# Performance work log

Hardware: AMD Instinct MI355X
Metric: run time of the kernel (lower is better)

## Reference

```python
import jax, jax.numpy as jnp
import numpy as np

VOCAB = 32000
D_MODEL = 768
D_FF = 3072
N_LAYERS = 12
SEQ = 2048
BATCH = 8
EPS = 1e-5  # torch LayerNorm default


def _layernorm(x, g, b):
    mu = jnp.mean(x, axis=-1, keepdims=True)
    var = jnp.mean(jnp.square(x - mu), axis=-1, keepdims=True)
    return (x - mu) * jax.lax.rsqrt(var + EPS) * g + b


def setup_inputs() -> dict:
    key = jax.random.key(0)
    ks = jax.random.split(key, 12)
    tokens = jax.random.randint(ks[0], (BATCH, SEQ), 0, VOCAB)
    embed = jax.random.normal(ks[1], (VOCAB, D_MODEL), dtype=jnp.float32) * 0.02
    ln1_g = jnp.ones((N_LAYERS, D_MODEL), dtype=jnp.float32)
    ln1_b = jnp.zeros((N_LAYERS, D_MODEL), dtype=jnp.float32)
    ln2_g = jnp.ones((N_LAYERS, D_MODEL), dtype=jnp.float32)
    ln2_b = jnp.zeros((N_LAYERS, D_MODEL), dtype=jnp.float32)
    W1 = jax.random.normal(ks[2], (N_LAYERS, D_MODEL, D_FF), dtype=jnp.float32) * (1.0 / np.sqrt(D_MODEL))
    b1 = jnp.zeros((N_LAYERS, D_FF), dtype=jnp.float32)
    W2 = jax.random.normal(ks[3], (N_LAYERS, D_FF, D_MODEL), dtype=jnp.float32) * (1.0 / np.sqrt(D_FF))
    b2 = jnp.zeros((N_LAYERS, D_MODEL), dtype=jnp.float32)
    Wout = jax.random.normal(ks[4], (D_MODEL, VOCAB), dtype=jnp.float32) * (1.0 / np.sqrt(D_MODEL))
    bout = jnp.zeros((VOCAB,), dtype=jnp.float32)
    return {"tokens": tokens, "embed": embed, "ln1_g": ln1_g, "ln1_b": ln1_b,
            "ln2_g": ln2_g, "ln2_b": ln2_b, "W1": W1, "b1": b1, "W2": W2, "b2": b2,
            "Wout": Wout, "bout": bout}


def reference(tokens, embed, ln1_g, ln1_b, ln2_g, ln2_b, W1, b1, W2, b2, Wout, bout):
    # embedding lookup; embed_size == d_model so projection is Identity.
    x = embed[tokens]  # [B, S, D]
    # dropout is inference-mode identity
    for l in range(N_LAYERS):
        res = x
        h = _layernorm(x, ln1_g[l], ln1_b[l])
        h = jnp.fft.fft2(h, axes=(-2, -1)).real  # token mixing, keep real part
        x = h + res
        res = x
        h = _layernorm(x, ln2_g[l], ln2_b[l])
        h = jax.nn.gelu(jnp.einsum('bsd,df->bsf', h, W1[l]) + b1[l], approximate=False)
        h = jnp.einsum('bsf,fd->bsd', h, W2[l]) + b2[l]
        x = h + res
    # predict from last position
    return jnp.einsum('bd,dv->bv', x[:, -1, :], Wout) + bout
```

## Files before the change

kernel.cpp:

```cpp
#include <hip/hip_runtime.h>
#include <hip/hip_bf16.h>

typedef unsigned short u16;
typedef unsigned long long u64;
typedef __attribute__((ext_vector_type(8))) __bf16 bf16x8;
typedef __attribute__((ext_vector_type(4))) float f32x4;
typedef __attribute__((ext_vector_type(4))) unsigned short u16x4;

#define BB 8
#define SS 2048
#define DD 768
#define DFF 3072
#define NL 12
#define ROWS (BB*SS)
#define VOC 32000

__device__ __forceinline__ u16 f2bf(float f){
  union { float f; unsigned u; } v; v.f = f;
  unsigned u = v.u;
  u += 0x7FFF + ((u >> 16) & 1);
  return (u16)(u >> 16);
}
__device__ __forceinline__ float bf2f(u16 b){
  union { unsigned u; float f; } v; v.u = ((unsigned)b) << 16; return v.f;
}

__global__ void k_embed(const int* __restrict__ tok, const float4* __restrict__ emb,
                        float4* __restrict__ x){
  int i = blockIdx.x*256 + threadIdx.x;
  if (i >= ROWS*192) return;
  int row = i/192, c = i - row*192;
  x[i] = emb[(long)tok[row]*192 + c];
}

__global__ void k_dftD(u16* __restrict__ out){
  int i = blockIdx.x*256 + threadIdx.x;
  if (i >= 1536*768) return;
  int n = i/768, k = i - n*768;
  int nn = (n < 768) ? n : n - 768;
  int m = (nn*k) % 768;
  float a = 2.0f*(float)m/768.0f;
  out[i] = f2bf((n < 768) ? cospif(a) : sinpif(a));
}

__global__ void k_dftS2(u16* __restrict__ out){
  int i = blockIdx.x*256 + threadIdx.x;
  if (i >= 2048*2048) return;
  int t = i >> 11, slot = i & 2047;
  int ss = (slot <= 1024) ? slot : slot - 1024;
  int m = (t*ss) & 2047;
  float a = (float)m * (1.0f/1024.0f);
  out[i] = f2bf((slot <= 1024) ? cospif(a) : -sinpif(a));
}

template<bool RES>
__global__ void k_ln1_fold(float* __restrict__ x, const u16* __restrict__ t4,
                           const float* __restrict__ bias,
                           const float* __restrict__ g, const float* __restrict__ b,
                           u16* __restrict__ hp, u16* __restrict__ hm){
  int gid = blockIdx.x*4 + (threadIdx.x >> 6);
  if (gid >= 8*1025) return;
  int bb = gid/1025, t = gid - bb*1025;
  int u = (2048 - t) & 2047;
  long rt = (long)bb*2048 + t, ru = (long)bb*2048 + u;
  int lane = threadIdx.x & 63;
  float vt[12], vu[12];
  #pragma unroll
  for (int j = 0; j < 12; j++){
    int e = lane + j*64;
    float a0 = x[rt*DD + e], a1 = x[ru*DD + e];
    if (RES){
      float bv = bias[e];
      a0 += bf2f(t4[rt*DD + e]) + bv;
      a1 += bf2f(t4[ru*DD + e]) + bv;
    }
    vt[j] = a0; vu[j] = a1;
  }
  float s0 = 0.f, s1 = 0.f;
  #pragma unroll
  for (int j = 0; j < 12; j++){ s0 += vt[j]; s1 += vu[j]; }
  #pragma unroll
  for (int o = 32; o > 0; o >>= 1){ s0 += __shfl_xor(s0, o); s1 += __shfl_xor(s1, o); }
  float mu0 = s0*(1.0f/768.0f), mu1 = s1*(1.0f/768.0f);
  float q0 = 0.f, q1 = 0.f;
  #pragma unroll
  for (int j = 0; j < 12; j++){ float d0 = vt[j]-mu0, d1 = vu[j]-mu1; q0 += d0*d0; q1 += d1*d1; }
  #pragma unroll
  for (int o = 32; o > 0; o >>= 1){ q0 += __shfl_xor(q0, o); q1 += __shfl_xor(q1, o); }
  float r0 = rsqrtf(q0*(1.0f/768.0f) + 1e-5f);
  float r1 = rsqrtf(q1*(1.0f/768.0f) + 1e-5f);
  const bool single = (t == 0) || (t == 1024);
  u16* hpr = hp + ((long)bb*1280 + t)*DD;
  u16* hmr = hm + ((long)bb*1024 + t)*DD;
  #pragma unroll
  for (int j = 0; j < 12; j++){
    int e = lane + j*64;
    if (RES){ x[rt*DD + e] = vt[j]; x[ru*DD + e] = vu[j]; }
    float ht = (vt[j]-mu0)*r0*g[e] + b[e];
    float hu = (vu[j]-mu1)*r1*g[e] + b[e];
    hpr[e] = f2bf(single ? ht : ht + hu);
    if (!single) hmr[e] = f2bf(ht - hu);
  }
}

__global__ void k_ln2_fuse(float* __restrict__ x, const u16* __restrict__ t2,
                           const float* __restrict__ g, const float* __restrict__ b,
                           u16* __restrict__ h){
  long row = (long)blockIdx.x*4 + (threadIdx.x >> 6);
  int lane = threadIdx.x & 63;
  float v[12];
  float s = 0.f;
  #pragma unroll
  for (int j = 0; j < 12; j++){
    int e = lane + j*64;
    float a = x[row*DD + e] + bf2f(t2[row*DD + e]);
    v[j] = a; s += a;
  }
  #pragma unroll
  for (int o = 32; o > 0; o >>= 1) s += __shfl_xor(s, o);
  float mu = s * (1.0f/768.0f);
  float q = 0.f;
  #pragma unroll
  for (int j = 0; j < 12; j++){ float d = v[j]-mu; q += d*d; }
  #pragma unroll
  for (int o = 32; o > 0; o >>= 1) q += __shfl_xor(q, o);
  float rs = rsqrtf(q * (1.0f/768.0f) + 1e-5f);
  #pragma unroll
  for (int j = 0; j < 12; j++){
    int e = lane + j*64;
    x[row*DD + e] = v[j];
    h[row*DD + e] = f2bf((v[j]-mu)*rs*g[e] + b[e]);
  }
}

__global__ void k_transpose_cvt(const float* __restrict__ src, u16* __restrict__ dst,
                                int R, int C){
  __shared__ float t[32][33];
  int bx = blockIdx.x*32, by = blockIdx.y*32;
  int tx = threadIdx.x, ty = threadIdx.y;
  #pragma unroll
  for (int i = 0; i < 4; i++) t[ty+i*8][tx] = src[(long)(by+ty+i*8)*C + bx+tx];
  __syncthreads();
  #pragma unroll
  for (int i = 0; i < 4; i++) dst[(long)(bx+ty+i*8)*R + by+tx] = f2bf(t[tx][ty+i*8]);
}

#define EPI_ADDX 1
#define EPI_GELU 2
#define EPI_OUTB 3

#define MFMA_Q(H, G, BF) do { \
  __builtin_amdgcn_s_setprio(1); \
  _Pragma("unroll") \
  for (int mm = 0; mm < 4; ++mm) \
    _Pragma("unroll") \
    for (int nn = 0; nn < 2; ++nn) \
      _Pragma("unroll") \
      for (int ks = 0; ks < 2; ++ks) \
        acc[((H)<<2)+mm][((G)<<1)+nn] = __builtin_amdgcn_mfma_f32_16x16x32_bf16( \
            aF[mm][ks], BF[nn][ks], acc[((H)<<2)+mm][((G)<<1)+nn], 0, 0, 0); \
  __builtin_amdgcn_s_setprio(0); \
} while(0)

#define GEMM_CORE_BODY \
  f32x4 acc[8][4] = {}; \
  bf16x8 aF[4][2], b0F[2][2], b1F[2][2]; \
  auto stage = [&](int tile){ \
    if (tile >= NT) return; \
    _Pragma("unroll") \
    for (int hh = 0; hh < 4; ++hh){ \
      const int isB   = ((hh + 1) >> 1) & 1; \
      const int rhalf = ((hh >> 1) & 1) << 7; \
      const u16* src = isB ? Bb : Ab; \
      const int rb = (isB ? bn : bm) + rhalf + sRow; \
      const u16* s0 = src + (long)rb * K + (tile << 6) + sCol; \
      u16* d0 = &lds[tile & 1][isB][rhalf + (wave << 3)][0]; \
      __builtin_amdgcn_global_load_lds((__attribute__((address_space(1))) void*)(s0), \
                                       (__attribute__((address_space(3))) void*)(d0), 16, 0, 0); \
      __builtin_amdgcn_global_load_lds((__attribute__((address_space(1))) void*)(s0 + ((long)K << 6)), \
                                       (__attribute__((address_space(3))) void*)(d0 + 64*64), 16, 0, 0); \
    } \
  }; \
  auto readA = [&](int c, int H){ \
    const u16* base = &lds[c][0][(H << 7) + (wm << 6)][0]; \
    _Pragma("unroll") \
    for (int mm = 0; mm < 4; ++mm) \
      _Pragma("unroll") \
      for (int ks = 0; ks < 2; ++ks) \
        aF[mm][ks] = *(const bf16x8*)&base[((mm<<4) + fr)*64 + (((ks<<5) + fks8) ^ swz)]; \
  }; \
  auto readB = [&](int c, int G, bf16x8 (&bF)[2][2]){ \
    const u16* base = &lds[c][1][(G << 7) + (wn << 5)][0]; \
    _Pragma("unroll") \
    for (int nn = 0; nn < 2; ++nn) \
      _Pragma("unroll") \
      for (int ks = 0; ks < 2; ++ks) \
        bF[nn][ks] = *(const bf16x8*)&base[((nn<<4) + fr)*64 + (((ks<<5) + fks8) ^ swz)]; \
  }; \
  stage(0); \
  __syncthreads(); \
  for (int T = 0; T < NT; ++T){ \
    stage(T + 1); \
    int c = T & 1; \
    readA(c, 0); readB(c, 0, b0F); \
    MFMA_Q(0, 0, b0F); \
    readB(c, 1, b1F); \
    MFMA_Q(0, 1, b1F); \
    readA(c, 1); \
    MFMA_Q(1, 1, b1F); \
    MFMA_Q(1, 0, b0F); \
    __syncthreads(); \
  }

template<int EPI>
__global__ __launch_bounds__(512, 2)
void k_gemm256(const u16* __restrict__ A, const u16* __restrict__ BT,
               int Nt, int N, int K, int NT, long aBS, long btBS, int rowOffPerZ,
               float* __restrict__ X, const float* __restrict__ bias,
               u16* __restrict__ OUT){
  __shared__ __align__(16) u16 lds[2][2][256][64];
  const int tid  = threadIdx.x;
  const int wave = tid >> 6, lane = tid & 63;
  const int wm = wave >> 2, wn = wave & 3;

  const int bz = blockIdx.z;
  const u16* Ab = A + (long)bz*aBS;
  const u16* Bb = BT + (long)bz*btBS;
  const int rowOff = bz*rowOffPerZ;

  const int nwg = gridDim.x;
  const int id  = blockIdx.x;
  const int sw  = (id & 7) * (nwg >> 3) + (id >> 3);
  const int bn = (sw % Nt) << 8;
  const int bm = (sw / Nt) << 8;

  const int fr   = lane & 15;
  const int fks8 = (lane >> 4) << 3;
  const int swz  = (fr & 7) << 3;
  const int sRow = (wave << 3) + (lane >> 3);
  const int sCol = ((lane & 7) ^ ((lane >> 3) & 7)) << 3;

  GEMM_CORE_BODY

  const int er = (lane >> 4) << 2, ec = lane & 15;
  #pragma unroll
  for (int mi = 0; mi < 8; ++mi){
    int row = bm + ((mi >> 2) << 7) + (wm << 6) + ((mi & 3) << 4) + er;
    #pragma unroll
    for (int ni = 0; ni < 4; ++ni){
      int col = bn + ((ni >> 1) << 7) + (wn << 5) + ((ni & 1) << 4) + ec;
      f32x4 v = acc[mi][ni];
      if constexpr (EPI == EPI_ADDX){
        float bv = bias ? bias[col] : 0.0f;
        #pragma unroll
        for (int r = 0; r < 4; r++)
          X[(long)(rowOff + row + r)*N + col] += v[r] + bv;
      } else if constexpr (EPI == EPI_OUTB){
        #pragma unroll
        for (int r = 0; r < 4; r++)
          OUT[(long)(rowOff + row + r)*N + col] = f2bf(v[r]);
      } else {
        float bv = bias[col];
        #pragma unroll
        for (int r = 0; r < 4; r++){
          float tt = v[r] + bv;
          OUT[(long)(row + r)*N + col] = f2bf(0.5f*tt*(1.0f + erff(tt*0.70710678118654752f)));
        }
      }
    }
  }
}

__global__ __launch_bounds__(512, 2)
void k_gemm1(const u16* __restrict__ hp, const u16* __restrict__ hm,
             const u16* __restrict__ dftD, u16* __restrict__ Ff){
  __shared__ __align__(16) u16 lds[2][2][256][64];
  const int tid  = threadIdx.x;
  const int wave = tid >> 6, lane = tid & 63;
  const int wm = wave >> 2, wn = wave & 3;

  const int K = 768, NT = 12;
  const int nwg = gridDim.x;
  const int id  = blockIdx.x;
  int sw  = (id & 7) * (nwg >> 3) + (id >> 3);
  const bool plus = (sw < 120);
  const u16* Ab;
  const u16* Bb;
  if (plus){ Ab = hp; Bb = dftD; }
  else     { sw -= 120; Ab = hm; Bb = dftD + 768*768; }
  const int bn = (sw % 3) << 8;
  const int bm = (sw / 3) << 8;

  const int fr   = lane & 15;
  const int fks8 = (lane >> 4) << 3;
  const int swz  = (fr & 7) << 3;
  const int sRow = (wave << 3) + (lane >> 3);
  const int sCol = ((lane & 7) ^ ((lane >> 3) & 7)) << 3;

  GEMM_CORE_BODY

  const int er = (lane >> 4) << 2, ec = lane & 15;
  #pragma unroll
  for (int mi = 0; mi < 8; ++mi){
    int row = bm + ((mi >> 2) << 7) + (wm << 6) + ((mi & 3) << 4) + er;
    #pragma unroll
    for (int ni = 0; ni < 4; ++ni){
      int col = bn + ((ni >> 1) << 7) + (wn << 5) + ((ni & 1) << 4) + ec;
      f32x4 v = acc[mi][ni];
      u16x4 pk;
      #pragma unroll
      for (int r = 0; r < 4; r++) pk[r] = f2bf(v[r]);
      if (plus){
        int b = row / 1280, t = row - b*1280;
        u16* dst = Ff + ((long)(b*768 + col))*2048 + t;
        if (t <= 1020)      *(u16x4*)dst = pk;
        else if (t == 1024) dst[0] = pk[0];
      } else {
        int b = row >> 10, t = row & 1023;
        u16* dst = Ff + ((long)(b*768 + col))*2048 + 1024 + t;
        if (t == 0){ dst[1] = pk[1]; dst[2] = pk[2]; dst[3] = pk[3]; }
        else        *(u16x4*)dst = pk;
      }
    }
  }
}

__global__ void k_logits(const float* __restrict__ x, const float* __restrict__ Wout,
                         const float* __restrict__ bout, float* __restrict__ out){
  __shared__ float xl[8][768];
  int tid = threadIdx.x;
  for (int i = tid; i < 8*768; i += 256){
    int b = i/768, d = i - b*768;
    xl[b][d] = x[((long)(b*2048 + 2047))*768 + d];
  }
  __syncthreads();
  int v = blockIdx.x*256 + tid;
  float acc[8];
  float bv = bout[v];
  #pragma unroll
  for (int b = 0; b < 8; b++) acc[b] = bv;
  for (int d = 0; d < 768; d++){
    float w = Wout[(long)d*VOC + v];
    #pragma unroll
    for (int b = 0; b < 8; b++) acc[b] += xl[b][d]*w;
  }
  #pragma unroll
  for (int b = 0; b < 8; b++) out[(long)b*VOC + v] = acc[b];
}

extern "C" void kernel_launch(void* const* d_in, const int* in_sizes, int n_in,
                              void* d_out, int out_size, void* d_ws, size_t ws_size,
                              hipStream_t stream){
  const int*   tokens = (const int*)d_in[0];
  const float* embed  = (const float*)d_in[1];
  const float* ln1_g  = (const float*)d_in[2];
  const float* ln1_b  = (const float*)d_in[3];
  const float* ln2_g  = (const float*)d_in[4];
  const float* ln2_b  = (const float*)d_in[5];
  const float* W1     = (const float*)d_in[6];
  const float* b1     = (const float*)d_in[7];
  const float* W2     = (const float*)d_in[8];
  const float* b2     = (const float*)d_in[9];
  const float* Wout   = (const float*)d_in[10];
  const float* bout   = (const float*)d_in[11];
  float* out = (float*)d_out;

  char* p = (char*)d_ws;
  size_t off = 0;
  auto alloc = [&](size_t bytes)->char*{
    char* r = p + off; off += (bytes + 255) & ~(size_t)255; return r;
  };
  float* x    = (float*)alloc((size_t)ROWS*DD*4);
  u16*   h    = (u16*)  alloc((size_t)ROWS*DD*2);
  u16*  gbuf  = (u16*)  alloc((size_t)ROWS*DFF*2);
  u16*  tmpO  = (u16*)  alloc((size_t)ROWS*DD*2);
  u16*  dftD  = (u16*)  alloc((size_t)1536*768*2);
  u16*  dftS2 = (u16*)  alloc((size_t)2048*2048*2);
  u16*  w1t   = (u16*)  alloc((size_t)DFF*DD*2);
  u16*  w2t   = (u16*)  alloc((size_t)DD*DFF*2);
  if (off > ws_size) return;
  u16* hp = gbuf;
  u16* hm = gbuf + (size_t)8*1280*768;
  u16* Ff = hm   + (size_t)8*1024*768;

  k_dftD<<<(1536*768+255)/256, 256, 0, stream>>>(dftD);
  k_dftS2<<<(2048*2048+255)/256, 256, 0, stream>>>(dftS2);
  k_embed<<<(ROWS*192+255)/256, 256, 0, stream>>>(tokens, (const float4*)embed, (float4*)x);

  for (int l = 0; l < NL; l++){
    if (l == 0)
      k_ln1_fold<false><<<2050, 256, 0, stream>>>(x, nullptr, nullptr,
          ln1_g + l*DD, ln1_b + l*DD, hp, hm);
    else
      k_ln1_fold<true><<<2050, 256, 0, stream>>>(x, tmpO, b2 + (l-1)*DD,
          ln1_g + l*DD, ln1_b + l*DD, hp, hm);
    k_gemm1<<<216, 512, 0, stream>>>(hp, hm, dftD, Ff);
    k_gemm256<EPI_OUTB><<<dim3(8*3, 1, 8), 512, 0, stream>>>(
        dftS2, Ff, 3, 768, 2048, 32, 0, (long)768*2048, 2048, nullptr, nullptr, tmpO);
    k_ln2_fuse<<<ROWS/4, 256, 0, stream>>>(x, tmpO, ln2_g + l*DD, ln2_b + l*DD, h);
    k_transpose_cvt<<<dim3(DFF/32, DD/32), dim3(32,8), 0, stream>>>(
        W1 + (long)l*DD*DFF, w1t, DD, DFF);
    k_transpose_cvt<<<dim3(DD/32, DFF/32), dim3(32,8), 0, stream>>>(
        W2 + (long)l*DFF*DD, w2t, DFF, DD);
    k_gemm256<EPI_GELU><<<64*12, 512, 0, stream>>>(
        h, w1t, 12, 3072, 768, 12, 0, 0, 0, nullptr, b1 + l*DFF, gbuf);
    if (l < NL-1)
      k_gemm256<EPI_OUTB><<<64*3, 512, 0, stream>>>(
          gbuf, w2t, 3, 768, 3072, 48, 0, 0, 0, nullptr, nullptr, tmpO);
    else
      k_gemm256<EPI_ADDX><<<64*3, 512, 0, stream>>>(
          gbuf, w2t, 3, 768, 3072, 48, 0, 0, 0, x, b2 + l*DD, nullptr);
  }
  k_logits<<<VOC/256, 256, 0, stream>>>(x, Wout, bout, out);
}
```

Measured before the change: 4.141 ms.

## Split-K the token-mixing and FFN-down GEMMs four ways, prune last layer

The DFT sequence-mixing GEMM and the W2 down-projection now split K four ways over blockIdx.y. Each slice writes a bf16 partial, and the four partials are summed inside the following LayerNorm kernels. For the last layer, only row 2047 of each batch is needed downstream, so its FFN and mixing GEMMs run on just the last 256-row tile and ln2 processes only 8 rows. The intent is better GPU occupancy for the small grids and less wasted work in the final layer. In exchange it adds partial-buffer traffic, an extra workspace, and bf16 rounding of each partial.

New measurement: 4.459 ms. 7.7% more time.

```diff
diff --git a/kernel.cpp b/kernel.cpp
--- a/kernel.cpp
+++ b/kernel.cpp
@@ -53,8 +53,10 @@
   out[i] = f2bf((slot <= 1024) ? cospif(a) : -sinpif(a));
 }
 
-template<bool RES>
-__global__ void k_ln1_fold(float* __restrict__ x, const u16* __restrict__ t4,
+template<bool RES, int NP>
+__global__ void k_ln1_fold(float* __restrict__ x,
+                           const u16* __restrict__ q0, const u16* __restrict__ q1,
+                           const u16* __restrict__ q2, const u16* __restrict__ q3,
                            const float* __restrict__ bias,
                            const float* __restrict__ g, const float* __restrict__ b,
                            u16* __restrict__ hp, u16* __restrict__ hm){
@@ -71,8 +73,12 @@
     float a0 = x[rt*DD + e], a1 = x[ru*DD + e];
     if (RES){
       float bv = bias[e];
-      a0 += bf2f(t4[rt*DD + e]) + bv;
-      a1 += bf2f(t4[ru*DD + e]) + bv;
+      a0 += bv + bf2f(q0[rt*DD + e]);
+      a1 += bv + bf2f(q0[ru*DD + e]);
+      if (NP == 4){
+        a0 += bf2f(q1[rt*DD + e]) + bf2f(q2[rt*DD + e]) + bf2f(q3[rt*DD + e]);
+        a1 += bf2f(q1[ru*DD + e]) + bf2f(q2[ru*DD + e]) + bf2f(q3[ru*DD + e]);
+      }
     }
     vt[j] = a0; vu[j] = a1;
   }
@@ -82,13 +88,13 @@
   #pragma unroll
   for (int o = 32; o > 0; o >>= 1){ s0 += __shfl_xor(s0, o); s1 += __shfl_xor(s1, o); }
   float mu0 = s0*(1.0f/768.0f), mu1 = s1*(1.0f/768.0f);
-  float q0 = 0.f, q1 = 0.f;
-  #pragma unroll
-  for (int j = 0; j < 12; j++){ float d0 = vt[j]-mu0, d1 = vu[j]-mu1; q0 += d0*d0; q1 += d1*d1; }
-  #pragma unroll
-  for (int o = 32; o > 0; o >>= 1){ q0 += __shfl_xor(q0, o); q1 += __shfl_xor(q1, o); }
-  float r0 = rsqrtf(q0*(1.0f/768.0f) + 1e-5f);
-  float r1 = rsqrtf(q1*(1.0f/768.0f) + 1e-5f);
+  float q0v = 0.f, q1v = 0.f;
+  #pragma unroll
+  for (int j = 0; j < 12; j++){ float d0 = vt[j]-mu0, d1 = vu[j]-mu1; q0v += d0*d0; q1v += d1*d1; }
+  #pragma unroll
+  for (int o = 32; o > 0; o >>= 1){ q0v += __shfl_xor(q0v, o); q1v += __shfl_xor(q1v, o); }
+  float r0 = rsqrtf(q0v*(1.0f/768.0f) + 1e-5f);
+  float r1 = rsqrtf(q1v*(1.0f/768.0f) + 1e-5f);
   const bool single = (t == 0) || (t == 1024);
   u16* hpr = hp + ((long)bb*1280 + t)*DD;
   u16* hmr = hm + ((long)bb*1024 + t)*DD;
@@ -103,17 +109,22 @@
   }
 }
 
-__global__ void k_ln2_fuse(float* __restrict__ x, const u16* __restrict__ t2,
+__global__ void k_ln2_fuse(float* __restrict__ x,
+                           const u16* __restrict__ p0, const u16* __restrict__ p1,
+                           const u16* __restrict__ p2, const u16* __restrict__ p3,
                            const float* __restrict__ g, const float* __restrict__ b,
-                           u16* __restrict__ h){
-  long row = (long)blockIdx.x*4 + (threadIdx.x >> 6);
+                           u16* __restrict__ h, int rmul, int radd, int nrows){
+  int gid = blockIdx.x*4 + (threadIdx.x >> 6);
+  if (gid >= nrows) return;
+  long row = (long)gid*rmul + radd;
   int lane = threadIdx.x & 63;
   float v[12];
   float s = 0.f;
   #pragma unroll
   for (int j = 0; j < 12; j++){
     int e = lane + j*64;
-    float a = x[row*DD + e] + bf2f(t2[row*DD + e]);
+    long ix = row*DD + e;
+    float a = x[ix] + bf2f(p0[ix]) + bf2f(p1[ix]) + bf2f(p2[ix]) + bf2f(p3[ix]);
     v[j] = a; s += a;
   }
   #pragma unroll
@@ -156,9 +167,9 @@
     _Pragma("unroll") \
     for (int nn = 0; nn < 2; ++nn) \
       _Pragma("unroll") \
-      for (int ks = 0; ks < 2; ++ks) \
+      for (int ks2 = 0; ks2 < 2; ++ks2) \
         acc[((H)<<2)+mm][((G)<<1)+nn] = __builtin_amdgcn_mfma_f32_16x16x32_bf16( \
-            aF[mm][ks], BF[nn][ks], acc[((H)<<2)+mm][((G)<<1)+nn], 0, 0, 0); \
+            aF[mm][ks2], BF[nn][ks2], acc[((H)<<2)+mm][((G)<<1)+nn], 0, 0, 0); \
   __builtin_amdgcn_s_setprio(0); \
 } while(0)
 
@@ -173,7 +184,7 @@
       const int rhalf = ((hh >> 1) & 1) << 7; \
       const u16* src = isB ? Bb : Ab; \
       const int rb = (isB ? bn : bm) + rhalf + sRow; \
-      const u16* s0 = src + (long)rb * K + (tile << 6) + sCol; \
+      const u16* s0 = src + (long)rb * K + koff + (tile << 6) + sCol; \
       u16* d0 = &lds[tile & 1][isB][rhalf + (wave << 3)][0]; \
       __builtin_amdgcn_global_load_lds((__attribute__((address_space(1))) void*)(s0), \
                                        (__attribute__((address_space(3))) void*)(d0), 16, 0, 0); \
@@ -186,16 +197,16 @@
     _Pragma("unroll") \
     for (int mm = 0; mm < 4; ++mm) \
       _Pragma("unroll") \
-      for (int ks = 0; ks < 2; ++ks) \
-        aF[mm][ks] = *(const bf16x8*)&base[((mm<<4) + fr)*64 + (((ks<<5) + fks8) ^ swz)]; \
+      for (int ks2 = 0; ks2 < 2; ++ks2) \
+        aF[mm][ks2] = *(const bf16x8*)&base[((mm<<4) + fr)*64 + (((ks2<<5) + fks8) ^ swz)]; \
   }; \
   auto readB = [&](int c, int G, bf16x8 (&bF)[2][2]){ \
     const u16* base = &lds[c][1][(G << 7) + (wn << 5)][0]; \
     _Pragma("unroll") \
     for (int nn = 0; nn < 2; ++nn) \
       _Pragma("unroll") \
-      for (int ks = 0; ks < 2; ++ks) \
-        bF[nn][ks] = *(const bf16x8*)&base[((nn<<4) + fr)*64 + (((ks<<5) + fks8) ^ swz)]; \
+      for (int ks2 = 0; ks2 < 2; ++ks2) \
+        bF[nn][ks2] = *(const bf16x8*)&base[((nn<<4) + fr)*64 + (((ks2<<5) + fks8) ^ swz)]; \
   }; \
   stage(0); \
   __syncthreads(); \
@@ -216,23 +227,28 @@
 __global__ __launch_bounds__(512, 2)
 void k_gemm256(const u16* __restrict__ A, const u16* __restrict__ BT,
                int Nt, int N, int K, int NT, long aBS, long btBS, int rowOffPerZ,
+               int mMul, int mAdd, int kStep,
                float* __restrict__ X, const float* __restrict__ bias,
-               u16* __restrict__ OUT){
+               u16* __restrict__ P0, u16* __restrict__ P1,
+               u16* __restrict__ P2, u16* __restrict__ P3){
   __shared__ __align__(16) u16 lds[2][2][256][64];
   const int tid  = threadIdx.x;
   const int wave = tid >> 6, lane = tid & 63;
   const int wm = wave >> 2, wn = wave & 3;
 
   const int bz = blockIdx.z;
+  const int ksl = blockIdx.y;
+  const long koff = (long)ksl * kStep;
+  u16* OUT = (ksl == 0) ? P0 : (ksl == 1) ? P1 : (ksl == 2) ? P2 : P3;
   const u16* Ab = A + (long)bz*aBS;
   const u16* Bb = BT + (long)bz*btBS;
   const int rowOff = bz*rowOffPerZ;
 
   const int nwg = gridDim.x;
   const int id  = blockIdx.x;
-  const int sw  = (id & 7) * (nwg >> 3) + (id >> 3);
+  const int sw  = ((nwg & 7) == 0) ? ((id & 7) * (nwg >> 3) + (id >> 3)) : id;
   const int bn = (sw % Nt) << 8;
-  const int bm = (sw / Nt) << 8;
+  const int bm = ((sw / Nt) * mMul + mAdd) << 8;
 
   const int fr   = lane & 15;
   const int fks8 = (lane >> 4) << 3;
@@ -280,6 +296,7 @@
   const int wm = wave >> 2, wn = wave & 3;
 
   const int K = 768, NT = 12;
+  const long koff = 0;
   const int nwg = gridDim.x;
   const int id  = blockIdx.x;
   int sw  = (id & 7) * (nwg >> 3) + (id >> 3);
@@ -379,37 +396,73 @@
   u16*  w1t   = (u16*)  alloc((size_t)DFF*DD*2);
   u16*  w2t   = (u16*)  alloc((size_t)DD*DFF*2);
   if (off > ws_size) return;
+  size_t offBase = off;
+  u16*  opt   = (u16*)  alloc((size_t)ROWS*DD*2*2);
+  const bool split4 = (off <= ws_size);
+  if (!split4) off = offBase;
+
   u16* hp = gbuf;
   u16* hm = gbuf + (size_t)8*1280*768;
   u16* Ff = hm   + (size_t)8*1024*768;
+  u16* gbT = gbuf + (size_t)26738688;
+  u16* opt2 = opt + (size_t)ROWS*DD;
 
   k_dftD<<<(1536*768+255)/256, 256, 0, stream>>>(dftD);
   k_dftS2<<<(2048*2048+255)/256, 256, 0, stream>>>(dftS2);
   k_embed<<<(ROWS*192+255)/256, 256, 0, stream>>>(tokens, (const float4*)embed, (float4*)x);
 
   for (int l = 0; l < NL; l++){
+    const bool last = (l == NL-1);
     if (l == 0)
-      k_ln1_fold<false><<<2050, 256, 0, stream>>>(x, nullptr, nullptr,
-          ln1_g + l*DD, ln1_b + l*DD, hp, hm);
+      k_ln1_fold<false,1><<<2050, 256, 0, stream>>>(x, nullptr, nullptr, nullptr, nullptr,
+          nullptr, ln1_g + l*DD, ln1_b + l*DD, hp, hm);
+    else if (split4)
+      k_ln1_fold<true,4><<<2050, 256, 0, stream>>>(x, tmpO, h, opt, opt2,
+          b2 + (l-1)*DD, ln1_g + l*DD, ln1_b + l*DD, hp, hm);
     else
-      k_ln1_fold<true><<<2050, 256, 0, stream>>>(x, tmpO, b2 + (l-1)*DD,
-          ln1_g + l*DD, ln1_b + l*DD, hp, hm);
+      k_ln1_fold<true,1><<<2050, 256, 0, stream>>>(x, tmpO, nullptr, nullptr, nullptr,
+          b2 + (l-1)*DD, ln1_g + l*DD, ln1_b + l*DD, hp, hm);
     k_gemm1<<<216, 512, 0, stream>>>(hp, hm, dftD, Ff);
-    k_gemm256<EPI_OUTB><<<dim3(8*3, 1, 8), 512, 0, stream>>>(
-        dftS2, Ff, 3, 768, 2048, 32, 0, (long)768*2048, 2048, nullptr, nullptr, tmpO);
-    k_ln2_fuse<<<ROWS/4, 256, 0, stream>>>(x, tmpO, ln2_g + l*DD, ln2_b + l*DD, h);
+    if (!last)
+      k_gemm256<EPI_OUTB><<<dim3(24, 4, 8), 512, 0, stream>>>(
+          dftS2, Ff, 3, 768, 2048, 8, 0, (long)768*2048, 2048, 1, 0, 512,
+          nullptr, nullptr, tmpO, h, gbuf, gbT);
+    else
+      k_gemm256<EPI_OUTB><<<dim3(3, 4, 8), 512, 0, stream>>>(
+          dftS2, Ff, 3, 768, 2048, 8, 0, (long)768*2048, 2048, 1, 7, 512,
+          nullptr, nullptr, tmpO, h, gbuf, gbT);
+    if (!last)
+      k_ln2_fuse<<<4096, 256, 0, stream>>>(x, tmpO, h, gbuf, gbT,
+          ln2_g + l*DD, ln2_b + l*DD, h, 1, 0, 16384);
+    else
+      k_ln2_fuse<<<2, 256, 0, stream>>>(x, tmpO, h, gbuf, gbT,
+          ln2_g + l*DD, ln2_b + l*DD, h, 2048, 2047, 8);
     k_transpose_cvt<<<dim3(DFF/32, DD/32), dim3(32,8), 0, stream>>>(
         W1 + (long)l*DD*DFF, w1t, DD, DFF);
     k_transpose_cvt<<<dim3(DD/32, DFF/32), dim3(32,8), 0, stream>>>(
         W2 + (long)l*DFF*DD, w2t, DFF, DD);
-    k_gemm256<EPI_GELU><<<64*12, 512, 0, stream>>>(
-        h, w1t, 12, 3072, 768, 12, 0, 0, 0, nullptr, b1 + l*DFF, gbuf);
-    if (l < NL-1)
-      k_gemm256<EPI_OUTB><<<64*3, 512, 0, stream>>>(
-          gbuf, w2t, 3, 768, 3072, 48, 0, 0, 0, nullptr, nullptr, tmpO);
+    if (!last)
+      k_gemm256<EPI_GELU><<<768, 512, 0, stream>>>(
+          h, w1t, 12, 3072, 768, 12, 0, 0, 0, 1, 0, 0,
+          nullptr, b1 + l*DFF, gbuf, nullptr, nullptr, nullptr);
     else
-      k_gemm256<EPI_ADDX><<<64*3, 512, 0, stream>>>(
-          gbuf, w2t, 3, 768, 3072, 48, 0, 0, 0, x, b2 + l*DD, nullptr);
+      k_gemm256<EPI_GELU><<<96, 512, 0, stream>>>(
+          h, w1t, 12, 3072, 768, 12, 0, 0, 0, 8, 7, 0,
+          nullptr, b1 + l*DFF, gbuf, nullptr, nullptr, nullptr);
+    if (!last){
+      if (split4)
+        k_gemm256<EPI_OUTB><<<dim3(192, 4, 1), 512, 0, stream>>>(
+            gbuf, w2t, 3, 768, 3072, 12, 0, 0, 0, 1, 0, 768,
+            nullptr, nullptr, tmpO, h, opt, opt2);
+      else
+        k_gemm256<EPI_OUTB><<<dim3(192, 1, 1), 512, 0, stream>>>(
+            gbuf, w2t, 3, 768, 3072, 48, 0, 0, 0, 1, 0, 0,
+            nullptr, nullptr, tmpO, nullptr, nullptr, nullptr);
+    } else {
+      k_gemm256<EPI_ADDX><<<dim3(24, 1, 1), 512, 0, stream>>>(
+          gbuf, w2t, 3, 768, 3072, 48, 0, 0, 0, 8, 7, 0,
+          x, b2 + l*DD, nullptr, nullptr, nullptr, nullptr);
+    }
   }
   k_logits<<<VOC/256, 256, 0, stream>>>(x, Wout, bout, out);
 }
```
